# Kernel tuning notes

Hardware: AMD Instinct MI355X
Metric: run time of the kernel (lower is better)

## Reference

```python
import jax, jax.numpy as jnp
import numpy as np


def setup_inputs() -> dict:
    key = jax.random.key(0)
    k1, k2, k3 = jax.random.split(key, 3)
    B, Tc, Tq, D = 8, 4096, 1024, 256
    context = jax.random.normal(k1, (B, Tc, D), dtype=jnp.float32)
    question = jax.random.normal(k2, (B, Tq, D), dtype=jnp.float32)
    w = jax.random.normal(k3, (3 * D, 1), dtype=jnp.float32) * 0.05
    return {"context": context, "question": question, "w": w}


def reference(context, question, w):
    # context: (B, Tc, D); question: (B, Tq, D); w: (3D, 1)
    D = context.shape[-1]
    w1, w2, w3 = w[:D, 0], w[D:2 * D, 0], w[2 * D:, 0]
    # Fused similarity: S[b,i,j] = w1.c_i + w2.q_j + w3.(c_i*q_j)
    # (mathematically identical to the tiled concat + linear score, but
    # avoids materializing the (B,Tc,Tq,3D) tensor)
    s_c = jnp.einsum('bid,d->bi', context, w1)              # (B, Tc)
    s_q = jnp.einsum('bjd,d->bj', question, w2)             # (B, Tq)
    s_cq = jnp.einsum('bid,bjd->bij', context * w3, question)  # (B, Tc, Tq)
    S = s_cq + s_c[:, :, None] + s_q[:, None, :]
    A = jax.nn.softmax(S, axis=-1)                           # (B, Tc, Tq)
    # C2Q attention: U[b,i] = sum_j A[b,i,j] * q_j
    U = jnp.einsum('bij,bjd->bid', A, question)              # (B, Tc, D)
    # Q2C attention: b_i = max_j A[b,i,j]; h = sum_i b_i * c_i, tiled over Tc
    b = jnp.max(A, axis=-1)                                  # (B, Tc)
    h = jnp.einsum('bi,bid->bd', b, context)                 # (B, D)
    H = jnp.broadcast_to(h[:, None, :], context.shape)       # (B, Tc, D)
    # megamerge
    G = jnp.concatenate([context, U, context * U, context * H], axis=-1)
    return G  # (B, Tc, 4D)
```

## Files before the change

### kernel.cpp

```cpp
#include <hip/hip_runtime.h>
#include <hip/hip_bf16.h>
#include <stdint.h>
#include <stddef.h>


#define NB 8
#define TC 4096
#define TQ 1024
#define DD 256
#define JT 32
#define NJT (TQ / JT)

typedef __attribute__((ext_vector_type(4)))  float  f32x4v;
typedef __attribute__((ext_vector_type(8)))  __bf16 bf16x8v;
typedef __attribute__((ext_vector_type(4)))  __bf16 bf16x4v;

#define QA_OFF   0
#define QX_OFF   (QA_OFF + NB*NJT*16*1024)
#define SQ_OFF   (QX_OFF + NB*NJT*16*1024)
#define BV_OFF   (SQ_OFF + NB*TQ*4)
#define HV_OFF   (BV_OFF + NB*TC*4)

__device__ __forceinline__ void async_cp16(const void* g, void* l) {
  __builtin_amdgcn_global_load_lds(
      (const __attribute__((address_space(1))) void*)g,
      (__attribute__((address_space(3))) void*)l, 16, 0, 0);
}

__global__ __launch_bounds__(256) void k_qprep(const float* __restrict__ question,
                                               const float* __restrict__ w,
                                               char* __restrict__ ws) {
  uint4* qa = (uint4*)(ws + QA_OFF);
  uint4* qx = (uint4*)(ws + QX_OFF);
  float* sq = (float*)(ws + SQ_OFF);
  __shared__ __align__(16) __bf16 T[32][264];

  int bx = blockIdx.x;
  int b = bx >> 5, it = bx & 31;
  int t = threadIdx.x;
  int j = t >> 3;
  int seg = t & 7;

  const float* qrow = question + ((size_t)(b * TQ + it * JT + j)) * DD + seg * 32;
  const float* w2 = w + DD;

  float part = 0.f;
#pragma unroll
  for (int k = 0; k < 8; ++k) {
    float4 v  = *(const float4*)(qrow + 4 * k);
    float4 wv = *(const float4*)(w2 + seg * 32 + 4 * k);
    part += v.x * wv.x + v.y * wv.y + v.z * wv.z + v.w * wv.w;
    bf16x4v pk = {(__bf16)v.x, (__bf16)v.y, (__bf16)v.z, (__bf16)v.w};
    *(bf16x4v*)&T[j][seg * 32 + 4 * k] = pk;
  }
  part += __shfl_xor(part, 1);
  part += __shfl_xor(part, 2);
  part += __shfl_xor(part, 4);
  if (seg == 0) sq[b * TQ + it * JT + j] = part;
  __syncthreads();

#pragma unroll
  for (int p = 0; p < 4; ++p) {
    int ch = t + 256 * p;
    int L = ch & 63, cc = ch >> 6;
    int jm = cc >> 3, c = cc & 7;
    int nh = L & 15, qh = L >> 4;
    uint4 v = *(const uint4*)&T[16 * jm + nh][32 * c + 8 * qh];
    qa[(size_t)(b * NJT + it) * 1024 + ch] = v;
  }
#pragma unroll
  for (int p = 0; p < 4; ++p) {
    int ch = t + 256 * p;
    int L = ch & 63, mt = ch >> 6;
    int nh = L & 15, qh = L >> 4;
    __bf16 e[8];
#pragma unroll
    for (int o = 0; o < 8; ++o) e[o] = T[8 * qh + o][16 * mt + nh];
    qx[(size_t)(b * NJT + it) * 1024 + ch] = *(const uint4*)e;
  }
}

__global__ __launch_bounds__(256, 2) void k_main(const float* __restrict__ context,
                                                 const float* __restrict__ w,
                                                 const char* __restrict__ ws,
                                                 float* __restrict__ bv_out,
                                                 float* __restrict__ out) {
  const uint4*  qa = (const uint4*)(ws + QA_OFF);
  const __bf16* qx = (const __bf16*)(ws + QX_OFF);
  const float*  sq = (const float*)(ws + SQ_OFF);

  __shared__ __align__(16) __bf16 qa_lds[2][8192];
  __shared__ __align__(16) __bf16 pa_lds[4][16][40];
  __shared__ __align__(16) float  sq_all[TQ];

  int bx = blockIdx.x;
  int b = bx & 7;
  int ig = bx >> 3;
  int t = threadIdx.x;
  int wv = t >> 6;
  int lane = t & 63;
  int nh = lane & 15;
  int qh = lane >> 4;
  int i0w = ig * 64 + wv * 16;

  const uint4* qa_b = qa + (size_t)b * NJT * 1024;
  const __bf16* qx_b = qx + (size_t)b * NJT * 8192;
  const float* sqb = sq + b * TQ;

  bf16x8v cw3f[8];
  {
    const float* crow = context + ((size_t)(b * TC + i0w + nh)) * DD;
    const float* w3 = w + 2 * DD;
#pragma unroll
    for (int c = 0; c < 8; ++c) {
      int d0 = 32 * c + 8 * qh;
      float4 f0 = *(const float4*)(crow + d0);
      float4 f1 = *(const float4*)(crow + d0 + 4);
      float4 g0 = *(const float4*)(w3 + d0);
      float4 g1 = *(const float4*)(w3 + d0 + 4);
      bf16x8v fr;
      fr[0] = (__bf16)(f0.x * g0.x); fr[1] = (__bf16)(f0.y * g0.y);
      fr[2] = (__bf16)(f0.z * g0.z); fr[3] = (__bf16)(f0.w * g0.w);
      fr[4] = (__bf16)(f1.x * g1.x); fr[5] = (__bf16)(f1.y * g1.y);
      fr[6] = (__bf16)(f1.z * g1.z); fr[7] = (__bf16)(f1.w * g1.w);
      cw3f[c] = fr;
    }
  }

  {
    ((float4*)sq_all)[t] = ((const float4*)sqb)[t];
    const uint4* src = qa_b;
#pragma unroll
    for (int p = 0; p < 4; ++p) {
      int cb = wv * 64 + p * 256;
      async_cp16(src + cb + lane, &qa_lds[0][(size_t)cb * 8]);
    }
  }

  f32x4v U[16];
#pragma unroll
  for (int mt = 0; mt < 16; ++mt) U[mt] = (f32x4v){0.f, 0.f, 0.f, 0.f};
  float m_run = -1e30f, l_run = 0.f;

  __syncthreads();

  for (int itq = 0; itq < NJT; ++itq) {
    int cur = itq & 1;

    if (itq + 1 < NJT) {
      const uint4* src = qa_b + (size_t)(itq + 1) * 1024;
#pragma unroll
      for (int p = 0; p < 4; ++p) {
        int cb = wv * 64 + p * 256;
        async_cp16(src + cb + lane, &qa_lds[cur ^ 1][(size_t)cb * 8]);
      }
    }

    f32x4v S0 = {0.f, 0.f, 0.f, 0.f}, S1 = {0.f, 0.f, 0.f, 0.f};
#pragma unroll
    for (int c = 0; c < 8; ++c) {
      bf16x8v a0 = *(const bf16x8v*)&qa_lds[cur][((0 * 8 + c) * 64 + lane) * 8];
      bf16x8v a1 = *(const bf16x8v*)&qa_lds[cur][((1 * 8 + c) * 64 + lane) * 8];
      S0 = __builtin_amdgcn_mfma_f32_16x16x32_bf16(a0, cw3f[c], S0, 0, 0, 0);
      S1 = __builtin_amdgcn_mfma_f32_16x16x32_bf16(a1, cw3f[c], S1, 0, 0, 0);
    }

    float4 sq0 = *(const float4*)&sq_all[itq * JT + 4 * qh];
    float4 sq1 = *(const float4*)&sq_all[itq * JT + 16 + 4 * qh];
    float e0 = __expf(S0[0] + sq0.x), e1 = __expf(S0[1] + sq0.y);
    float e2 = __expf(S0[2] + sq0.z), e3 = __expf(S0[3] + sq0.w);
    float f0 = __expf(S1[0] + sq1.x), f1 = __expf(S1[1] + sq1.y);
    float f2 = __expf(S1[2] + sq1.z), f3 = __expf(S1[3] + sq1.w);
    float v0 = fmaxf(fmaxf(S0[0] + sq0.x, S0[1] + sq0.y), fmaxf(S0[2] + sq0.z, S0[3] + sq0.w));
    float v1 = fmaxf(fmaxf(S1[0] + sq1.x, S1[1] + sq1.y), fmaxf(S1[2] + sq1.z, S1[3] + sq1.w));
    m_run = fmaxf(m_run, fmaxf(v0, v1));
    l_run += ((e0 + e1) + (e2 + e3)) + ((f0 + f1) + (f2 + f3));

    bf16x4v pk0 = {(__bf16)e0, (__bf16)e1, (__bf16)e2, (__bf16)e3};
    bf16x4v pk1 = {(__bf16)f0, (__bf16)f1, (__bf16)f2, (__bf16)f3};
    *(bf16x4v*)&pa_lds[wv][nh][4 * qh]      = pk0;
    *(bf16x4v*)&pa_lds[wv][nh][16 + 4 * qh] = pk1;

    bf16x8v af = *(const bf16x8v*)&pa_lds[wv][nh][8 * qh];

    const __bf16* qxt = qx_b + (size_t)itq * 8192 + lane * 8;
#pragma unroll
    for (int mt = 0; mt < 16; ++mt) {
      bf16x8v bq = *(const bf16x8v*)(qxt + mt * 512);
      U[mt] = __builtin_amdgcn_mfma_f32_16x16x32_bf16(af, bq, U[mt], 0, 0, 0);
    }

    __syncthreads();
  }

  float lo = l_run + __shfl_xor(l_run, 16);
  lo += __shfl_xor(lo, 32);
  float mo = fmaxf(m_run, __shfl_xor(m_run, 16));
  mo = fmaxf(mo, __shfl_xor(mo, 32));
  float rinv = 1.0f / lo;
  if ((t & 63) < 16) bv_out[b * TC + i0w + nh] = __expf(mo) * rinv;

  float rv[4];
#pragma unroll
  for (int r = 0; r < 4; ++r) rv[r] = __shfl(rinv, 4 * qh + r);

#pragma unroll
  for (int r = 0; r < 4; ++r) {
    int ig_row = i0w + 4 * qh + r;
    const float* crow = context + ((size_t)(b * TC + ig_row)) * DD;
    float* orow = out + ((size_t)(b * TC + ig_row)) * (4 * DD);
#pragma unroll
    for (int mt = 0; mt < 16; ++mt) {
      int d = 16 * mt + nh;
      float c = crow[d];
      float u = U[mt][r] * rv[r];
      orow[d] = c;
      orow[DD + d] = u;
      orow[2 * DD + d] = c * u;
    }
  }
}

__global__ __launch_bounds__(256) void k_hred(const float* __restrict__ context,
                                              const char* __restrict__ ws,
                                              float* __restrict__ hv) {
  const float* bv = (const float*)(ws + BV_OFF);
  __shared__ float bsh[128];
  int bx = blockIdx.x;
  int b = bx >> 5, ch = bx & 31;
  int i0 = ch * 128;
  int t = threadIdx.x;
  if (t < 128) bsh[t] = bv[b * TC + i0 + t];
  __syncthreads();
  float acc = 0.f;
  const float* cp = context + ((size_t)(b * TC + i0)) * DD + t;
#pragma unroll 4
  for (int r = 0; r < 128; ++r) acc += bsh[r] * cp[(size_t)r * DD];
  atomicAdd(&hv[b * DD + t], acc);
}

__global__ __launch_bounds__(256) void k_final(const float* __restrict__ context,
                                               const char* __restrict__ ws,
                                               float* __restrict__ out) {
  const float* hv = (const float*)(ws + HV_OFF);
  int gid = blockIdx.x * 256 + threadIdx.x;
  int row = gid >> 6;
  int d = (gid & 63) * 4;
  int b = row >> 12;
  float4 c4 = ((const float4*)context)[gid];
  float4 h4 = *(const float4*)(hv + b * DD + d);
  float4 r;
  r.x = c4.x * h4.x; r.y = c4.y * h4.y; r.z = c4.z * h4.z; r.w = c4.w * h4.w;
  *(float4*)(out + (size_t)row * TQ + 3 * DD + d) = r;
}

extern "C" void kernel_launch(void* const* d_in, const int* in_sizes, int n_in,
                              void* d_out, int out_size, void* d_ws, size_t ws_size,
                              hipStream_t stream) {
  (void)in_sizes; (void)n_in; (void)out_size; (void)ws_size;
  const float* context  = (const float*)d_in[0];
  const float* question = (const float*)d_in[1];
  const float* w        = (const float*)d_in[2];
  float* out = (float*)d_out;
  char* ws = (char*)d_ws;

  k_qprep<<<NB * NJT, 256, 0, stream>>>(question, w, ws);
  k_main<<<NB * (TC / 64), 256, 0, stream>>>(context, w, ws,
                                             (float*)(ws + BV_OFF), out);
  hipMemsetAsync(ws + HV_OFF, 0, NB * DD * sizeof(float), stream);
  k_hred<<<NB * 32, 256, 0, stream>>>(context, ws, (float*)(ws + HV_OFF));
  k_final<<<(NB * TC * DD / 4) / 256, 256, 0, stream>>>(context, ws, out);
}
```

Baseline: 232.8 us.

## Split PV matmul across waves by D columns, sharing P tiles via LDS

The P·Q matmul is repartitioned. Before, each wave loaded all 16 D-column fragments of Q from global memory for its own 16 rows. Now each wave loads only its 4 D-column fragments and computes all 64 rows of the block by reading every wave's P tile from LDS after a barrier. This cuts per-wave global/L2 traffic for the Q tile by four, at the cost of an extra barrier per iteration. Row normalization factors are shared through LDS for the new epilogue mapping.

After: 225.0 us. -3.4%, faster.

```diff
diff --git a/kernel.cpp b/kernel.cpp
--- a/kernel.cpp
+++ b/kernel.cpp
@@ -92,6 +92,7 @@
   __shared__ __align__(16) __bf16 qa_lds[2][8192];
   __shared__ __align__(16) __bf16 pa_lds[4][16][40];
   __shared__ __align__(16) float  sq_all[TQ];
+  __shared__ __align__(16) float  rinv_lds[64];
 
   int bx = blockIdx.x;
   int b = bx & 7;
@@ -139,7 +140,7 @@
 
   f32x4v U[16];
 #pragma unroll
-  for (int mt = 0; mt < 16; ++mt) U[mt] = (f32x4v){0.f, 0.f, 0.f, 0.f};
+  for (int k = 0; k < 16; ++k) U[k] = (f32x4v){0.f, 0.f, 0.f, 0.f};
   float m_run = -1e30f, l_run = 0.f;
 
   __syncthreads();
@@ -163,6 +164,14 @@
       bf16x8v a1 = *(const bf16x8v*)&qa_lds[cur][((1 * 8 + c) * 64 + lane) * 8];
       S0 = __builtin_amdgcn_mfma_f32_16x16x32_bf16(a0, cw3f[c], S0, 0, 0, 0);
       S1 = __builtin_amdgcn_mfma_f32_16x16x32_bf16(a1, cw3f[c], S1, 0, 0, 0);
+    }
+
+    bf16x8v bqr[4];
+    {
+      const __bf16* qxt = qx_b + (size_t)itq * 8192 + lane * 8;
+#pragma unroll
+      for (int nt = 0; nt < 4; ++nt)
+        bqr[nt] = *(const bf16x8v*)(qxt + (size_t)(wv * 4 + nt) * 512);
     }
 
     float4 sq0 = *(const float4*)&sq_all[itq * JT + 4 * qh];
@@ -181,13 +190,14 @@
     *(bf16x4v*)&pa_lds[wv][nh][4 * qh]      = pk0;
     *(bf16x4v*)&pa_lds[wv][nh][16 + 4 * qh] = pk1;
 
-    bf16x8v af = *(const bf16x8v*)&pa_lds[wv][nh][8 * qh];
-
-    const __bf16* qxt = qx_b + (size_t)itq * 8192 + lane * 8;
-#pragma unroll
-    for (int mt = 0; mt < 16; ++mt) {
-      bf16x8v bq = *(const bf16x8v*)(qxt + mt * 512);
-      U[mt] = __builtin_amdgcn_mfma_f32_16x16x32_bf16(af, bq, U[mt], 0, 0, 0);
+    asm volatile("s_waitcnt lgkmcnt(0)\n\ts_barrier" ::: "memory");
+
+#pragma unroll
+    for (int mi = 0; mi < 4; ++mi) {
+      bf16x8v af = *(const bf16x8v*)&pa_lds[mi][nh][8 * qh];
+#pragma unroll
+      for (int nt = 0; nt < 4; ++nt)
+        U[mi * 4 + nt] = __builtin_amdgcn_mfma_f32_16x16x32_bf16(af, bqr[nt], U[mi * 4 + nt], 0, 0, 0);
     }
 
     __syncthreads();
@@ -198,25 +208,29 @@
   float mo = fmaxf(m_run, __shfl_xor(m_run, 16));
   mo = fmaxf(mo, __shfl_xor(mo, 32));
   float rinv = 1.0f / lo;
-  if ((t & 63) < 16) bv_out[b * TC + i0w + nh] = __expf(mo) * rinv;
-
-  float rv[4];
-#pragma unroll
-  for (int r = 0; r < 4; ++r) rv[r] = __shfl(rinv, 4 * qh + r);
-
-#pragma unroll
-  for (int r = 0; r < 4; ++r) {
-    int ig_row = i0w + 4 * qh + r;
-    const float* crow = context + ((size_t)(b * TC + ig_row)) * DD;
-    float* orow = out + ((size_t)(b * TC + ig_row)) * (4 * DD);
-#pragma unroll
-    for (int mt = 0; mt < 16; ++mt) {
-      int d = 16 * mt + nh;
-      float c = crow[d];
-      float u = U[mt][r] * rv[r];
-      orow[d] = c;
-      orow[DD + d] = u;
-      orow[2 * DD + d] = c * u;
+  if (lane < 16) {
+    bv_out[b * TC + i0w + nh] = __expf(mo) * rinv;
+    rinv_lds[wv * 16 + nh] = rinv;
+  }
+  __syncthreads();
+
+#pragma unroll
+  for (int mi = 0; mi < 4; ++mi) {
+#pragma unroll
+    for (int r = 0; r < 4; ++r) {
+      int row = ig * 64 + mi * 16 + 4 * qh + r;
+      float rv = rinv_lds[mi * 16 + 4 * qh + r];
+      const float* crow = context + ((size_t)(b * TC + row)) * DD;
+      float* orow = out + ((size_t)(b * TC + row)) * (4 * DD);
+#pragma unroll
+      for (int nt = 0; nt < 4; ++nt) {
+        int d = wv * 64 + nt * 16 + nh;
+        float c = crow[d];
+        float u = U[mi * 4 + nt][r] * rv;
+        orow[d] = c;
+        orow[DD + d] = u;
+        orow[2 * DD + d] = c * u;
+      }
     }
   }
 }
```
